# Kernel optimization log

Hardware: AMD Instinct MI355X
Metric: run time of the kernel (lower is better)

## Reference

```python
import jax, jax.numpy as jnp
import numpy as np

B, T, D, H = 64, 512, 512, 1024


def setup_inputs() -> dict:
    key = jax.random.key(0)
    k1, k2, k3 = jax.random.split(key, 3)
    x = jax.random.normal(k1, (B, T, D), dtype=jnp.float32)
    W = jax.random.normal(k2, (D, 4 * H), dtype=jnp.float32) * 0.02  # input kernel
    U = jax.random.normal(k3, (H, 4 * H), dtype=jnp.float32) * 0.02  # recurrent kernel
    b = jnp.zeros((4 * H,), dtype=jnp.float32)
    return {"x": x, "W": W, "U": U, "b": b}


def reference(x, W, U, b):
    # Keras LSTM, gate order [i, f, c(g), o], sigmoid recurrent activation, tanh activation.
    # return_sequences=False, return_state=True -> pred == h_T; output = concat([h_T, h_T, c_T]).
    batch = x.shape[0]
    hidden = U.shape[0]

    def step(carry, xt):
        h, c = carry
        z = xt @ W + h @ U + b  # [B, 4H]
        i, f, g, o = jnp.split(z, 4, axis=-1)
        i = jax.nn.sigmoid(i)
        f = jax.nn.sigmoid(f)
        o = jax.nn.sigmoid(o)
        c_new = f * c + i * jnp.tanh(g)
        h_new = o * jnp.tanh(c_new)
        return (h_new, c_new), None

    h0 = jnp.zeros((batch, hidden), dtype=x.dtype)
    c0 = jnp.zeros((batch, hidden), dtype=x.dtype)
    xs = jnp.swapaxes(x, 0, 1)  # [T, B, D]
    (hT, cT), _ = jax.lax.scan(step, (h0, c0), xs)
    return jnp.concatenate([hT, hT, cT], axis=-1)  # [B, 3H]
```

## Files before the change

kernel.cpp:

```cpp
#include <hip/hip_runtime.h>
#include <stdint.h>

typedef unsigned short u16;

#define T_STEPS 512
#define BATCH   64
#define DIN     512
#define HID     1024
#define G4      4096
#define NBLK    128
#define NH      8
#define NC      32
#define THREADS 512

#define U_LD    1032
#define W_LD    520

#define SM_BYTES 99328
#define WT_OFF   66048

#define XB_BYTES ((size_t)T_STEPS * BATCH * DIN * 2)
#define HB_OFF   XB_BYTES
#define HB_BYTES (2u * BATCH * HID * 2)
#define FLG_OFF  (HB_OFF + HB_BYTES)
#define FLG_BYTES 2048
#define WS_NEED  (FLG_OFF + FLG_BYTES)

typedef float f32x16 __attribute__((ext_vector_type(16)));
typedef short bf16x8 __attribute__((ext_vector_type(8)));
typedef unsigned uint32x4 __attribute__((ext_vector_type(4)));

__device__ __forceinline__ u16 f2bf(float f) {
  unsigned u = __float_as_uint(f);
  u += 0x7fffu + ((u >> 16) & 1u);
  return (u16)(u >> 16);
}
__device__ __forceinline__ float sigm(float x) {
  return __builtin_amdgcn_rcpf(1.f + __expf(-x));
}
__device__ __forceinline__ float fast_tanh(float x) {
  return 1.f - 2.f * __builtin_amdgcn_rcpf(__expf(2.f * x) + 1.f);
}

__device__ __forceinline__ uint32x4 load16_sc(uint64_t addr) {
  uint32x4 d;
  asm volatile("global_load_dwordx4 %0, %1, off sc0 sc1" : "=v"(d) : "v"(addr));
  return d;
}
__device__ __forceinline__ unsigned load4_sc(uint64_t addr) {
  unsigned d;
  asm volatile("global_load_dword %0, %1, off sc0 sc1" : "=v"(d) : "v"(addr));
  return d;
}
__device__ __forceinline__ void store16_sc(uint64_t addr, uint32x4 v) {
  asm volatile("global_store_dwordx4 %0, %1, off sc0 sc1" :: "v"(addr), "v"(v) : "memory");
}
__device__ __forceinline__ void store4_sc(uint64_t addr, unsigned v) {
  asm volatile("global_store_dword %0, %1, off sc0 sc1" :: "v"(addr), "v"(v) : "memory");
}
#define WAITV(n) asm volatile("s_waitcnt vmcnt(" #n ")" ::: "memory")

__global__ void cvt_x(const float* __restrict__ x, u16* __restrict__ xb) {
  int i = blockIdx.x * 256 + threadIdx.x;
  int dblk = i & 63;
  int rest = i >> 6;
  int b = rest & 63;
  int t = rest >> 6;
  const float4* s = reinterpret_cast<const float4*>(x + ((size_t)(b * T_STEPS + t)) * DIN + dblk * 8);
  float4 f0 = s[0], f1 = s[1];
  uint4 o;
  o.x = (unsigned)f2bf(f0.x) | ((unsigned)f2bf(f0.y) << 16);
  o.y = (unsigned)f2bf(f0.z) | ((unsigned)f2bf(f0.w) << 16);
  o.z = (unsigned)f2bf(f1.x) | ((unsigned)f2bf(f1.y) << 16);
  o.w = (unsigned)f2bf(f1.z) | ((unsigned)f2bf(f1.w) << 16);
  *reinterpret_cast<uint4*>(xb + ((size_t)(t * BATCH + b)) * DIN + dblk * 8) = o;
}

__launch_bounds__(THREADS)
__global__ void lstm_kernel(const float* __restrict__ W, const float* __restrict__ U,
                            const float* __restrict__ bias, const u16* __restrict__ xb,
                            u16* __restrict__ hbuf, float* __restrict__ out,
                            unsigned* __restrict__ flags) {
  __shared__ __align__(16) char smraw[SM_BYTES];
  u16* Ut = (u16*)smraw;
  u16* Wt = (u16*)(smraw + WT_OFF);
  float* zp = (float*)smraw;

  const int tid = threadIdx.x;
  const int bid = blockIdx.x;
  const int j0 = bid * NH;

  for (int idx = tid; idx < NC * HID; idx += THREADS) {
    int c = idx & (NC - 1);
    int k = idx >> 5;
    int gcol = ((c >> 3) << 10) + j0 + (c & 7);
    Ut[c * U_LD + k] = f2bf(U[(size_t)k * G4 + gcol]);
  }
  for (int idx = tid; idx < NC * DIN; idx += THREADS) {
    int c = idx & (NC - 1);
    int k = idx >> 5;
    int gcol = ((c >> 3) << 10) + j0 + (c & 7);
    Wt[c * W_LD + k] = f2bf(W[(size_t)k * G4 + gcol]);
  }
  __syncthreads();

  const int l   = tid & 63;
  const int wv  = tid >> 6;
  const int m_t = wv & 1;
  const int ks  = wv >> 1;
  const int cl  = l & 31;
  const int q   = l >> 5;

  bf16x8 ubf[16], wbf[8];
  {
    const u16* ub = Ut + cl * U_LD + ks * 256 + q * 8;
#pragma unroll
    for (int s = 0; s < 16; ++s) ubf[s] = *(const bf16x8*)(ub + s * 16);
    const u16* wb = Wt + cl * W_LD + ks * 128 + q * 8;
#pragma unroll
    for (int s = 0; s < 8; ++s) wbf[s] = *(const bf16x8*)(wb + s * 16);
  }
  __syncthreads();

  const int row = m_t * 32 + cl;
  const int pb = tid >> 3;
  const int pu = tid & 7;
  float c_reg = 0.f;
  const float bi  = bias[j0 + pu];
  const float bf_ = bias[1024 + j0 + pu];
  const float bg  = bias[2048 + j0 + pu];
  const float bo  = bias[3072 + j0 + pu];

  const uint64_t fbase = (uint64_t)flags;
  const uint64_t faddr = fbase + (uint64_t)(ks * 32 + cl) * 16;
  const uint64_t hlane = (uint64_t)(ks * 32 + q) * 1024 + (uint64_t)row * 16;
  const uint64_t puboff = (uint64_t)bid * 1024 + (uint64_t)(wv * 8 + (l >> 3)) * 16;

#define HMFMA(S) acc = __builtin_amdgcn_mfma_f32_32x32x16_bf16( \
    __builtin_bit_cast(bf16x8, abuf[S]), ubf[S], acc, 0, 0, 0)

  for (int t = 0; t < T_STEPS; ++t) {
    f32x16 acc = {0.f,0.f,0.f,0.f,0.f,0.f,0.f,0.f,0.f,0.f,0.f,0.f,0.f,0.f,0.f,0.f};

    const u16* xa = xb + (size_t)t * (BATCH * DIN) + row * DIN + ks * 128 + q * 8;
#pragma unroll
    for (int s = 0; s < 8; ++s) {
      bf16x8 av = *(const bf16x8*)(xa + s * 16);
      acc = __builtin_amdgcn_mfma_f32_32x32x16_bf16(av, wbf[s], acc, 0, 0, 0);
    }

    while (true) {
      unsigned f = load4_sc(faddr);
      WAITV(0);
      if (__all(f >= (unsigned)t)) break;
      __builtin_amdgcn_s_sleep(1);
    }

    const uint64_t hb = (uint64_t)hbuf + (uint64_t)(t & 1) * (BATCH * HID * 2) + hlane;
    uint32x4 abuf[16];
#pragma unroll
    for (int s = 0; s < 16; ++s) abuf[s] = load16_sc(hb + (uint64_t)s * 2048);
    WAITV(12); __builtin_amdgcn_sched_barrier(0);
    HMFMA(0); HMFMA(1); HMFMA(2); HMFMA(3);
    WAITV(8); __builtin_amdgcn_sched_barrier(0);
    HMFMA(4); HMFMA(5); HMFMA(6); HMFMA(7);
    WAITV(4); __builtin_amdgcn_sched_barrier(0);
    HMFMA(8); HMFMA(9); HMFMA(10); HMFMA(11);
    WAITV(0); __builtin_amdgcn_sched_barrier(0);
    HMFMA(12); HMFMA(13); HMFMA(14); HMFMA(15);

#pragma unroll
    for (int r = 0; r < 16; ++r) {
      int rl = (r & 3) + 8 * (r >> 2) + 4 * q;
      zp[ks * 2112 + (m_t * 32 + rl) * 33 + cl] = acc[r];
    }
    __syncthreads();

    float zi = bi, zf = bf_, zg = bg, zo = bo;
#pragma unroll
    for (int k2 = 0; k2 < 4; ++k2) {
      const float* zr = zp + k2 * 2112 + pb * 33;
      zi += zr[pu]; zf += zr[pu + 8]; zg += zr[pu + 16]; zo += zr[pu + 24];
    }
    float ig = sigm(zi), fg = sigm(zf), og = sigm(zo);
    float gg = fast_tanh(zg);
    c_reg = fg * c_reg + ig * gg;
    float h = og * fast_tanh(c_reg);

    unsigned hval = (unsigned)f2bf(h);
    unsigned other = __shfl_xor(hval, 1);
    unsigned pair32 = (l & 1) ? ((other & 0xffffu) | (hval << 16))
                              : ((hval & 0xffffu) | (other << 16));
    int base = l & ~7;
    uint32x4 hv;
    hv[0] = __shfl(pair32, base);
    hv[1] = __shfl(pair32, base + 2);
    hv[2] = __shfl(pair32, base + 4);
    hv[3] = __shfl(pair32, base + 6);

    const uint64_t hbn = (uint64_t)hbuf + (uint64_t)((t + 1) & 1) * (BATCH * HID * 2);
    if ((l & 7) == 0) store16_sc(hbn + puboff, hv);
    if (t == T_STEPS - 1) {
      float* orow = out + (size_t)pb * 3072 + j0 + pu;
      orow[0]    = h;
      orow[1024] = h;
      orow[2048] = c_reg;
    }
    WAITV(0);
    __syncthreads();
    if (tid == 0) store4_sc(fbase + (uint64_t)bid * 16, (unsigned)(t + 1));
  }
#undef HMFMA
}

extern "C" void kernel_launch(void* const* d_in, const int* in_sizes, int n_in,
                              void* d_out, int out_size, void* d_ws, size_t ws_size,
                              hipStream_t stream) {
  const float* x = (const float*)d_in[0];
  const float* W = (const float*)d_in[1];
  const float* U = (const float*)d_in[2];
  const float* b = (const float*)d_in[3];
  float* out = (float*)d_out;

  if (ws_size < WS_NEED) return;

  u16* xb         = (u16*)d_ws;
  u16* hbuf       = (u16*)((char*)d_ws + HB_OFF);
  unsigned* flags = (unsigned*)((char*)d_ws + FLG_OFF);

  hipMemsetAsync((void*)hbuf, 0, HB_BYTES + FLG_BYTES, stream);
  cvt_x<<<(T_STEPS * BATCH * DIN / 8 + 255) / 256, 256, 0, stream>>>(x, xb);
  lstm_kernel<<<NBLK, THREADS, 0, stream>>>(W, U, b, xb, hbuf, out, flags);
}
```

Before: 2.584 ms.

## Split batch into two halves and pipeline LSTM steps across them

Splits the 64-row batch into two independent 32-row chunks, each with its own h double buffer and per-wave flags. While one chunk's gate math and h publish run, the other chunk's h and x operands are already being prefetched, so cross-block wait latency overlaps with useful work. The K dimension is now split across all 8 waves instead of 4 waves times 2 M tiles. Gate columns are reinterleaved so the reduction can use float4 LDS reads. The spin loop gains a timeout escape that silently produces wrong results if it trips.

Result: slower. 2.644 ms (+2.3%).

```diff
diff --git a/kernel.cpp b/kernel.cpp
--- a/kernel.cpp
+++ b/kernel.cpp
@@ -21,9 +21,9 @@
 
 #define XB_BYTES ((size_t)T_STEPS * BATCH * DIN * 2)
 #define HB_OFF   XB_BYTES
-#define HB_BYTES (2u * BATCH * HID * 2)
+#define HB_BYTES (2u * 2u * 128 * 32 * 8 * 2)
 #define FLG_OFF  (HB_OFF + HB_BYTES)
-#define FLG_BYTES 2048
+#define FLG_BYTES (2 * 128 * 4 * 16)
 #define WS_NEED  (FLG_OFF + FLG_BYTES)
 
 typedef float f32x16 __attribute__((ext_vector_type(16)));
@@ -47,6 +47,11 @@
   asm volatile("global_load_dwordx4 %0, %1, off sc0 sc1" : "=v"(d) : "v"(addr));
   return d;
 }
+__device__ __forceinline__ uint32x4 load16_plain(uint64_t addr) {
+  uint32x4 d;
+  asm volatile("global_load_dwordx4 %0, %1, off" : "=v"(d) : "v"(addr));
+  return d;
+}
 __device__ __forceinline__ unsigned load4_sc(uint64_t addr) {
   unsigned d;
   asm volatile("global_load_dword %0, %1, off sc0 sc1" : "=v"(d) : "v"(addr));
@@ -59,6 +64,7 @@
   asm volatile("global_store_dword %0, %1, off sc0 sc1" :: "v"(addr), "v"(v) : "memory");
 }
 #define WAITV(n) asm volatile("s_waitcnt vmcnt(" #n ")" ::: "memory")
+#define SBAR()   __builtin_amdgcn_sched_barrier(0)
 
 __global__ void cvt_x(const float* __restrict__ x, u16* __restrict__ xb) {
   int i = blockIdx.x * 256 + threadIdx.x;
@@ -79,12 +85,11 @@
 __launch_bounds__(THREADS)
 __global__ void lstm_kernel(const float* __restrict__ W, const float* __restrict__ U,
                             const float* __restrict__ bias, const u16* __restrict__ xb,
-                            u16* __restrict__ hbuf, float* __restrict__ out,
-                            unsigned* __restrict__ flags) {
+                            char* __restrict__ ws, float* __restrict__ out) {
   __shared__ __align__(16) char smraw[SM_BYTES];
   u16* Ut = (u16*)smraw;
   u16* Wt = (u16*)(smraw + WT_OFF);
-  float* zp = (float*)smraw;
+  float (*zp)[32][36] = (float(*)[32][36])smraw;
 
   const int tid = threadIdx.x;
   const int bid = blockIdx.x;
@@ -93,124 +98,141 @@
   for (int idx = tid; idx < NC * HID; idx += THREADS) {
     int c = idx & (NC - 1);
     int k = idx >> 5;
-    int gcol = ((c >> 3) << 10) + j0 + (c & 7);
+    int gcol = ((c & 3) << 10) + j0 + (c >> 2);
     Ut[c * U_LD + k] = f2bf(U[(size_t)k * G4 + gcol]);
   }
   for (int idx = tid; idx < NC * DIN; idx += THREADS) {
     int c = idx & (NC - 1);
     int k = idx >> 5;
-    int gcol = ((c >> 3) << 10) + j0 + (c & 7);
+    int gcol = ((c & 3) << 10) + j0 + (c >> 2);
     Wt[c * W_LD + k] = f2bf(W[(size_t)k * G4 + gcol]);
   }
   __syncthreads();
 
-  const int l   = tid & 63;
-  const int wv  = tid >> 6;
-  const int m_t = wv & 1;
-  const int ks  = wv >> 1;
-  const int cl  = l & 31;
-  const int q   = l >> 5;
-
-  bf16x8 ubf[16], wbf[8];
+  const int l  = tid & 63;
+  const int wv = tid >> 6;
+  const int cl = l & 31;
+  const int q  = l >> 5;
+
+  bf16x8 ubf[8], wbf[4];
   {
-    const u16* ub = Ut + cl * U_LD + ks * 256 + q * 8;
-#pragma unroll
-    for (int s = 0; s < 16; ++s) ubf[s] = *(const bf16x8*)(ub + s * 16);
-    const u16* wb = Wt + cl * W_LD + ks * 128 + q * 8;
-#pragma unroll
-    for (int s = 0; s < 8; ++s) wbf[s] = *(const bf16x8*)(wb + s * 16);
+    const u16* ub = Ut + cl * U_LD + wv * 128 + q * 8;
+#pragma unroll
+    for (int s = 0; s < 8; ++s) ubf[s] = *(const bf16x8*)(ub + s * 16);
+    const u16* wb = Wt + cl * W_LD + wv * 64 + q * 8;
+#pragma unroll
+    for (int s = 0; s < 4; ++s) wbf[s] = *(const bf16x8*)(wb + s * 16);
   }
   __syncthreads();
 
-  const int row = m_t * 32 + cl;
   const int pb = tid >> 3;
   const int pu = tid & 7;
-  float c_reg = 0.f;
   const float bi  = bias[j0 + pu];
   const float bf_ = bias[1024 + j0 + pu];
   const float bg  = bias[2048 + j0 + pu];
   const float bo  = bias[3072 + j0 + pu];
-
-  const uint64_t fbase = (uint64_t)flags;
-  const uint64_t faddr = fbase + (uint64_t)(ks * 32 + cl) * 16;
-  const uint64_t hlane = (uint64_t)(ks * 32 + q) * 1024 + (uint64_t)row * 16;
-  const uint64_t puboff = (uint64_t)bid * 1024 + (uint64_t)(wv * 8 + (l >> 3)) * 16;
-
-#define HMFMA(S) acc = __builtin_amdgcn_mfma_f32_32x32x16_bf16( \
-    __builtin_bit_cast(bf16x8, abuf[S]), ubf[S], acc, 0, 0, 0)
+  float cA = 0.f, cB = 0.f;
+  int alive = 1;
+
+  const uint64_t hbase = (uint64_t)ws + HB_OFF;
+  const uint64_t fbase = (uint64_t)ws + FLG_OFF;
+  const uint64_t xb64  = (uint64_t)xb;
+
+  uint32x4 hA[8], xA[4], hB[8], xB[4];
+
+  {
+    const uint64_t hbp = hbase + (uint64_t)cl * 16;
+#pragma unroll
+    for (int s = 0; s < 8; ++s) hA[s] = load16_sc(hbp + (uint64_t)((wv * 16 + 2 * s + q) * 32) * 16);
+    const uint64_t xap = xb64 + ((uint64_t)cl * 512 + (uint64_t)(wv * 64 + q * 8)) * 2;
+#pragma unroll
+    for (int s = 0; s < 4; ++s) xA[s] = load16_plain(xap + (uint64_t)s * 32);
+  }
+
+#define HMFMA(BUF, S) acc = __builtin_amdgcn_mfma_f32_32x32x16_bf16( \
+    __builtin_bit_cast(bf16x8, BUF[S]), ubf[S], acc, 0, 0, 0)
+#define XMFMA(BUF, S) acc = __builtin_amdgcn_mfma_f32_32x32x16_bf16( \
+    __builtin_bit_cast(bf16x8, BUF[S]), wbf[S], acc, 0, 0, 0)
+
+#define PHASE(CH, TT, HC, XC, HN, XN, CREG, OCH, OT) do {                        \
+    WAITV(0); SBAR();             \
+    f32x16 acc = {0.f,0.f,0.f,0.f,0.f,0.f,0.f,0.f,0.f,0.f,0.f,0.f,0.f,0.f,0.f,0.f}; \
+    HMFMA(HC,0); HMFMA(HC,1); HMFMA(HC,2); HMFMA(HC,3);                          \
+    HMFMA(HC,4); HMFMA(HC,5); HMFMA(HC,6); HMFMA(HC,7);                          \
+    XMFMA(XC,0); XMFMA(XC,1); XMFMA(XC,2); XMFMA(XC,3);                          \
+    _Pragma("unroll")                                                            \
+    for (int r = 0; r < 16; ++r) {                                               \
+      int rl = (r & 3) + 8 * (r >> 2) + 4 * q;                                   \
+      zp[wv][rl][cl] = acc[r];                                                   \
+    }                                                                            \
+    __syncthreads();                                   \
+    if (tid < 256) {                                                             \
+      float zi = bi, zf = bf_, zg = bg, zo = bo;                                 \
+      _Pragma("unroll")                                                          \
+      for (int k2 = 0; k2 < 8; ++k2) {                                           \
+        float4 v = *(const float4*)&zp[k2][pb][pu * 4];                          \
+        zi += v.x; zf += v.y; zg += v.z; zo += v.w;                              \
+      }                                                                          \
+      float ig = sigm(zi), fg = sigm(zf), og = sigm(zo);                         \
+      float gg = fast_tanh(zg);                                                  \
+      CREG = fg * CREG + ig * gg;                                                \
+      float h = og * fast_tanh(CREG);                                            \
+      unsigned hval = (unsigned)f2bf(h);                                         \
+      unsigned other = __shfl_xor(hval, 1);                                      \
+      unsigned pair32 = (l & 1) ? ((other & 0xffffu) | (hval << 16))             \
+                                : ((hval & 0xffffu) | (other << 16));            \
+      int base_ = l & ~7;                                                        \
+      uint32x4 hv;                                                               \
+      hv[0] = __shfl(pair32, base_);     hv[1] = __shfl(pair32, base_ + 2);      \
+      hv[2] = __shfl(pair32, base_ + 4); hv[3] = __shfl(pair32, base_ + 6);      \
+      if ((l & 7) == 0)                                                          \
+        store16_sc(hbase + (uint64_t)(CH) * 131072 +                             \
+                   (uint64_t)(((TT) + 1) & 1) * 65536 + (uint64_t)bid * 512 +    \
+                   (uint64_t)(wv * 8 + (l >> 3)) * 16, hv);                      \
+      if ((TT) == T_STEPS - 1) {                                                 \
+        float* orow = out + (size_t)((CH) * 32 + pb) * 3072 + j0 + pu;           \
+        orow[0] = h; orow[1024] = h; orow[2048] = CREG;                          \
+      }                                                                          \
+      WAITV(0);                        \
+      if (l == 0)                                                                \
+        store4_sc(fbase + (uint64_t)(CH) * 8192 + (uint64_t)bid * 64 +           \
+                  (uint64_t)wv * 16, (unsigned)((TT) + 1));                      \
+    }                                                                            \
+    if (alive) {                      \
+      const uint64_t fa = fbase + (uint64_t)(OCH) * 8192 +                       \
+                          (uint64_t)(wv * 16 + (l >> 2)) * 64 +                  \
+                          (uint64_t)(l & 3) * 16;                                \
+      int spins = 0;                                                             \
+      while (true) {                                                             \
+        unsigned f = load4_sc(fa);                                               \
+        WAITV(0);                                                                \
+        if (__all(f >= (unsigned)(OT))) break;                                   \
+        if (++spins > (1 << 22)) { alive = 0; break; }                           \
+        __builtin_amdgcn_s_sleep(1);                                             \
+      }                                                                          \
+    }                                                                            \
+    {                                 \
+      const uint64_t hbp = hbase + (uint64_t)(OCH) * 131072 +                    \
+                           (uint64_t)((OT) & 1) * 65536 + (uint64_t)cl * 16;     \
+      _Pragma("unroll")                                                          \
+      for (int s = 0; s < 8; ++s)                                                \
+        HN[s] = load16_sc(hbp + (uint64_t)((wv * 16 + 2 * s + q) * 32) * 16);    \
+      const int otx = ((OT) < T_STEPS) ? (OT) : 0;                               \
+      const uint64_t xap = xb64 + ((uint64_t)(otx * 64 + (OCH) * 32 + cl) * 512  \
+                                   + (uint64_t)(wv * 64 + q * 8)) * 2;           \
+      _Pragma("unroll")                                                          \
+      for (int s = 0; s < 4; ++s) XN[s] = load16_plain(xap + (uint64_t)s * 32);  \
+    }                                                                            \
+    __syncthreads();                              \
+  } while (0)
 
   for (int t = 0; t < T_STEPS; ++t) {
-    f32x16 acc = {0.f,0.f,0.f,0.f,0.f,0.f,0.f,0.f,0.f,0.f,0.f,0.f,0.f,0.f,0.f,0.f};
-
-    const u16* xa = xb + (size_t)t * (BATCH * DIN) + row * DIN + ks * 128 + q * 8;
-#pragma unroll
-    for (int s = 0; s < 8; ++s) {
-      bf16x8 av = *(const bf16x8*)(xa + s * 16);
-      acc = __builtin_amdgcn_mfma_f32_32x32x16_bf16(av, wbf[s], acc, 0, 0, 0);
-    }
-
-    while (true) {
-      unsigned f = load4_sc(faddr);
-      WAITV(0);
-      if (__all(f >= (unsigned)t)) break;
-      __builtin_amdgcn_s_sleep(1);
-    }
-
-    const uint64_t hb = (uint64_t)hbuf + (uint64_t)(t & 1) * (BATCH * HID * 2) + hlane;
-    uint32x4 abuf[16];
-#pragma unroll
-    for (int s = 0; s < 16; ++s) abuf[s] = load16_sc(hb + (uint64_t)s * 2048);
-    WAITV(12); __builtin_amdgcn_sched_barrier(0);
-    HMFMA(0); HMFMA(1); HMFMA(2); HMFMA(3);
-    WAITV(8); __builtin_amdgcn_sched_barrier(0);
-    HMFMA(4); HMFMA(5); HMFMA(6); HMFMA(7);
-    WAITV(4); __builtin_amdgcn_sched_barrier(0);
-    HMFMA(8); HMFMA(9); HMFMA(10); HMFMA(11);
-    WAITV(0); __builtin_amdgcn_sched_barrier(0);
-    HMFMA(12); HMFMA(13); HMFMA(14); HMFMA(15);
-
-#pragma unroll
-    for (int r = 0; r < 16; ++r) {
-      int rl = (r & 3) + 8 * (r >> 2) + 4 * q;
-      zp[ks * 2112 + (m_t * 32 + rl) * 33 + cl] = acc[r];
-    }
-    __syncthreads();
-
-    float zi = bi, zf = bf_, zg = bg, zo = bo;
-#pragma unroll
-    for (int k2 = 0; k2 < 4; ++k2) {
-      const float* zr = zp + k2 * 2112 + pb * 33;
-      zi += zr[pu]; zf += zr[pu + 8]; zg += zr[pu + 16]; zo += zr[pu + 24];
-    }
-    float ig = sigm(zi), fg = sigm(zf), og = sigm(zo);
-    float gg = fast_tanh(zg);
-    c_reg = fg * c_reg + ig * gg;
-    float h = og * fast_tanh(c_reg);
-
-    unsigned hval = (unsigned)f2bf(h);
-    unsigned other = __shfl_xor(hval, 1);
-    unsigned pair32 = (l & 1) ? ((other & 0xffffu) | (hval << 16))
-                              : ((hval & 0xffffu) | (other << 16));
-    int base = l & ~7;
-    uint32x4 hv;
-    hv[0] = __shfl(pair32, base);
-    hv[1] = __shfl(pair32, base + 2);
-    hv[2] = __shfl(pair32, base + 4);
-    hv[3] = __shfl(pair32, base + 6);
-
-    const uint64_t hbn = (uint64_t)hbuf + (uint64_t)((t + 1) & 1) * (BATCH * HID * 2);
-    if ((l & 7) == 0) store16_sc(hbn + puboff, hv);
-    if (t == T_STEPS - 1) {
-      float* orow = out + (size_t)pb * 3072 + j0 + pu;
-      orow[0]    = h;
-      orow[1024] = h;
-      orow[2048] = c_reg;
-    }
-    WAITV(0);
-    __syncthreads();
-    if (tid == 0) store4_sc(fbase + (uint64_t)bid * 16, (unsigned)(t + 1));
-  }
+    PHASE(0, t, hA, xA, hB, xB, cA, 1, t);
+    PHASE(1, t, hB, xB, hA, xA, cB, 0, t + 1);
+  }
+#undef PHASE
 #undef HMFMA
+#undef XMFMA
 }
 
 extern "C" void kernel_launch(void* const* d_in, const int* in_sizes, int n_in,
@@ -224,11 +246,8 @@
 
   if (ws_size < WS_NEED) return;
 
-  u16* xb         = (u16*)d_ws;
-  u16* hbuf       = (u16*)((char*)d_ws + HB_OFF);
-  unsigned* flags = (unsigned*)((char*)d_ws + FLG_OFF);
-
-  hipMemsetAsync((void*)hbuf, 0, HB_BYTES + FLG_BYTES, stream);
+  u16* xb = (u16*)d_ws;
+  hipMemsetAsync((char*)d_ws + HB_OFF, 0, HB_BYTES + FLG_BYTES, stream);
   cvt_x<<<(T_STEPS * BATCH * DIN / 8 + 255) / 256, 256, 0, stream>>>(x, xb);
-  lstm_kernel<<<NBLK, THREADS, 0, stream>>>(W, U, b, xb, hbuf, out, flags);
-}
+  lstm_kernel<<<NBLK, THREADS, 0, stream>>>(W, U, b, xb, (char*)d_ws, out);
+}
```

## Replace flag-based step barrier with step-tagged h values polled directly

Applied to the files above, without the earlier changes.

Drops the separate per-block flag array and its flag store and poll. Each bf16 h value is now packed with a 16-bit step tag into a 32-bit word, and consumers poll the h buffer itself until every tag matches, so the data and the readiness signal arrive in a single load round trip. The recurrent U fragments are no longer held in registers; they are read from LDS on every step, which frees registers for the doubled h load, and the z scratch area moves so it does not overwrite Ut. The cost is twice the h traffic per step, repeated reloads of the full h tile while spinning, extra LDS reads, and a spin limit that gives up silently instead of waiting forever.

New measurement: 5.586 ms. 2.16x slower.

```diff
diff --git a/kernel.cpp b/kernel.cpp
--- a/kernel.cpp
+++ b/kernel.cpp
@@ -16,15 +16,14 @@
 #define U_LD    1032
 #define W_LD    520
 
-#define SM_BYTES 99328
+#define SM_BYTES 99840
 #define WT_OFF   66048
 
 #define XB_BYTES ((size_t)T_STEPS * BATCH * DIN * 2)
 #define HB_OFF   XB_BYTES
-#define HB_BYTES (2u * BATCH * HID * 2)
-#define FLG_OFF  (HB_OFF + HB_BYTES)
-#define FLG_BYTES 2048
-#define WS_NEED  (FLG_OFF + FLG_BYTES)
+#define HB_PAR   262144
+#define HB_BYTES (2u * HB_PAR)
+#define WS_NEED  (HB_OFF + HB_BYTES)
 
 typedef float f32x16 __attribute__((ext_vector_type(16)));
 typedef short bf16x8 __attribute__((ext_vector_type(8)));
@@ -47,18 +46,16 @@
   asm volatile("global_load_dwordx4 %0, %1, off sc0 sc1" : "=v"(d) : "v"(addr));
   return d;
 }
-__device__ __forceinline__ unsigned load4_sc(uint64_t addr) {
-  unsigned d;
-  asm volatile("global_load_dword %0, %1, off sc0 sc1" : "=v"(d) : "v"(addr));
+__device__ __forceinline__ uint32x4 load16_plain(uint64_t addr) {
+  uint32x4 d;
+  asm volatile("global_load_dwordx4 %0, %1, off" : "=v"(d) : "v"(addr));
   return d;
 }
 __device__ __forceinline__ void store16_sc(uint64_t addr, uint32x4 v) {
   asm volatile("global_store_dwordx4 %0, %1, off sc0 sc1" :: "v"(addr), "v"(v) : "memory");
 }
-__device__ __forceinline__ void store4_sc(uint64_t addr, unsigned v) {
-  asm volatile("global_store_dword %0, %1, off sc0 sc1" :: "v"(addr), "v"(v) : "memory");
-}
 #define WAITV(n) asm volatile("s_waitcnt vmcnt(" #n ")" ::: "memory")
+#define SBAR()   __builtin_amdgcn_sched_barrier(0)
 
 __global__ void cvt_x(const float* __restrict__ x, u16* __restrict__ xb) {
   int i = blockIdx.x * 256 + threadIdx.x;
@@ -79,12 +76,11 @@
 __launch_bounds__(THREADS)
 __global__ void lstm_kernel(const float* __restrict__ W, const float* __restrict__ U,
                             const float* __restrict__ bias, const u16* __restrict__ xb,
-                            u16* __restrict__ hbuf, float* __restrict__ out,
-                            unsigned* __restrict__ flags) {
+                            char* __restrict__ ws, float* __restrict__ out) {
   __shared__ __align__(16) char smraw[SM_BYTES];
   u16* Ut = (u16*)smraw;
   u16* Wt = (u16*)(smraw + WT_OFF);
-  float* zp = (float*)smraw;
+  float* zp = (float*)(smraw + WT_OFF);
 
   const int tid = threadIdx.x;
   const int bid = blockIdx.x;
@@ -111,16 +107,15 @@
   const int cl  = l & 31;
   const int q   = l >> 5;
 
-  bf16x8 ubf[16], wbf[8];
+  bf16x8 wbf[8];
   {
-    const u16* ub = Ut + cl * U_LD + ks * 256 + q * 8;
-#pragma unroll
-    for (int s = 0; s < 16; ++s) ubf[s] = *(const bf16x8*)(ub + s * 16);
     const u16* wb = Wt + cl * W_LD + ks * 128 + q * 8;
 #pragma unroll
     for (int s = 0; s < 8; ++s) wbf[s] = *(const bf16x8*)(wb + s * 16);
   }
   __syncthreads();
+
+  const u16* ubp = Ut + cl * U_LD + ks * 256 + q * 8;
 
   const int row = m_t * 32 + cl;
   const int pb = tid >> 3;
@@ -131,43 +126,64 @@
   const float bg  = bias[2048 + j0 + pu];
   const float bo  = bias[3072 + j0 + pu];
 
-  const uint64_t fbase = (uint64_t)flags;
-  const uint64_t faddr = fbase + (uint64_t)(ks * 32 + cl) * 16;
-  const uint64_t hlane = (uint64_t)(ks * 32 + q) * 1024 + (uint64_t)row * 16;
-  const uint64_t puboff = (uint64_t)bid * 1024 + (uint64_t)(wv * 8 + (l >> 3)) * 16;
-
-#define HMFMA(S) acc = __builtin_amdgcn_mfma_f32_32x32x16_bf16( \
-    __builtin_bit_cast(bf16x8, abuf[S]), ubf[S], acc, 0, 0, 0)
+  const uint64_t hbB = (uint64_t)ws + HB_OFF;
+  const uint64_t xb64 = (uint64_t)xb;
+  const uint64_t hoff = (uint64_t)(ks * 32 + q) * 2048 + (uint64_t)row * 32;
+  const uint64_t puboff = (uint64_t)bid * 2048 + (uint64_t)(tid >> 3) * 32 +
+                          (uint64_t)((l >> 2) & 1) * 16;
+
+  int alive = 1;
 
   for (int t = 0; t < T_STEPS; ++t) {
+    const unsigned tagv = (unsigned)t;
+    const uint64_t hb = hbB + (uint64_t)(t & 1) * HB_PAR + hoff;
+
+    uint32x4 hbuf[32];
+#define ISSUEH() do { _Pragma("unroll") for (int s_ = 0; s_ < 16; ++s_) { \
+      hbuf[2 * s_]     = load16_sc(hb + (uint64_t)s_ * 4096); \
+      hbuf[2 * s_ + 1] = load16_sc(hb + (uint64_t)s_ * 4096 + 16); } } while (0)
+    ISSUEH();
+    uint32x4 xr[8];
+    {
+      const uint64_t xa = xb64 + ((uint64_t)t * (BATCH * DIN) +
+                                  (uint64_t)row * DIN + ks * 128 + q * 8) * 2;
+#pragma unroll
+      for (int s = 0; s < 8; ++s) xr[s] = load16_plain(xa + (uint64_t)s * 32);
+    }
+
+    int spins = 0;
+    while (alive) {
+      WAITV(0); SBAR();
+      unsigned bad = 0;
+#pragma unroll
+      for (int s = 0; s < 32; ++s) {
+#pragma unroll
+        for (int e = 0; e < 4; ++e) bad |= (hbuf[s][e] ^ tagv) & 0xffffu;
+      }
+      if (__all(bad == 0)) break;
+      if (++spins > (1 << 18)) { alive = 0; break; }
+      __builtin_amdgcn_s_sleep(4);
+      ISSUEH();
+    }
+#undef ISSUEH
+
     f32x16 acc = {0.f,0.f,0.f,0.f,0.f,0.f,0.f,0.f,0.f,0.f,0.f,0.f,0.f,0.f,0.f,0.f};
-
-    const u16* xa = xb + (size_t)t * (BATCH * DIN) + row * DIN + ks * 128 + q * 8;
-#pragma unroll
-    for (int s = 0; s < 8; ++s) {
-      bf16x8 av = *(const bf16x8*)(xa + s * 16);
-      acc = __builtin_amdgcn_mfma_f32_32x32x16_bf16(av, wbf[s], acc, 0, 0, 0);
-    }
-
-    while (true) {
-      unsigned f = load4_sc(faddr);
-      WAITV(0);
-      if (__all(f >= (unsigned)t)) break;
-      __builtin_amdgcn_s_sleep(1);
-    }
-
-    const uint64_t hb = (uint64_t)hbuf + (uint64_t)(t & 1) * (BATCH * HID * 2) + hlane;
-    uint32x4 abuf[16];
-#pragma unroll
-    for (int s = 0; s < 16; ++s) abuf[s] = load16_sc(hb + (uint64_t)s * 2048);
-    WAITV(12); __builtin_amdgcn_sched_barrier(0);
-    HMFMA(0); HMFMA(1); HMFMA(2); HMFMA(3);
-    WAITV(8); __builtin_amdgcn_sched_barrier(0);
-    HMFMA(4); HMFMA(5); HMFMA(6); HMFMA(7);
-    WAITV(4); __builtin_amdgcn_sched_barrier(0);
-    HMFMA(8); HMFMA(9); HMFMA(10); HMFMA(11);
-    WAITV(0); __builtin_amdgcn_sched_barrier(0);
-    HMFMA(12); HMFMA(13); HMFMA(14); HMFMA(15);
+#pragma unroll
+    for (int s = 0; s < 16; ++s) {
+      uint32x4 d0 = hbuf[2 * s], d1 = hbuf[2 * s + 1];
+      uint32x4 pk;
+      pk[0] = (d0[0] >> 16) | (d0[1] & 0xffff0000u);
+      pk[1] = (d0[2] >> 16) | (d0[3] & 0xffff0000u);
+      pk[2] = (d1[0] >> 16) | (d1[1] & 0xffff0000u);
+      pk[3] = (d1[2] >> 16) | (d1[3] & 0xffff0000u);
+      bf16x8 a = __builtin_bit_cast(bf16x8, pk);
+      bf16x8 uf = *(const bf16x8*)(ubp + s * 16);
+      acc = __builtin_amdgcn_mfma_f32_32x32x16_bf16(a, uf, acc, 0, 0, 0);
+    }
+#pragma unroll
+    for (int s = 0; s < 8; ++s)
+      acc = __builtin_amdgcn_mfma_f32_32x32x16_bf16(
+          __builtin_bit_cast(bf16x8, xr[s]), wbf[s], acc, 0, 0, 0);
 
 #pragma unroll
     for (int r = 0; r < 16; ++r) {
@@ -187,30 +203,24 @@
     c_reg = fg * c_reg + ig * gg;
     float h = og * fast_tanh(c_reg);
 
-    unsigned hval = (unsigned)f2bf(h);
-    unsigned other = __shfl_xor(hval, 1);
-    unsigned pair32 = (l & 1) ? ((other & 0xffffu) | (hval << 16))
-                              : ((hval & 0xffffu) | (other << 16));
-    int base = l & ~7;
+    unsigned hval = ((unsigned)f2bf(h) << 16) | (unsigned)(t + 1);
+    int base_ = l & ~3;
     uint32x4 hv;
-    hv[0] = __shfl(pair32, base);
-    hv[1] = __shfl(pair32, base + 2);
-    hv[2] = __shfl(pair32, base + 4);
-    hv[3] = __shfl(pair32, base + 6);
-
-    const uint64_t hbn = (uint64_t)hbuf + (uint64_t)((t + 1) & 1) * (BATCH * HID * 2);
-    if ((l & 7) == 0) store16_sc(hbn + puboff, hv);
+    hv[0] = __shfl(hval, base_);
+    hv[1] = __shfl(hval, base_ + 1);
+    hv[2] = __shfl(hval, base_ + 2);
+    hv[3] = __shfl(hval, base_ + 3);
+    if ((l & 3) == 0)
+      store16_sc(hbB + (uint64_t)((t + 1) & 1) * HB_PAR + puboff, hv);
+
     if (t == T_STEPS - 1) {
       float* orow = out + (size_t)pb * 3072 + j0 + pu;
       orow[0]    = h;
       orow[1024] = h;
       orow[2048] = c_reg;
     }
-    WAITV(0);
     __syncthreads();
-    if (tid == 0) store4_sc(fbase + (uint64_t)bid * 16, (unsigned)(t + 1));
-  }
-#undef HMFMA
+  }
 }
 
 extern "C" void kernel_launch(void* const* d_in, const int* in_sizes, int n_in,
@@ -224,11 +234,8 @@
 
   if (ws_size < WS_NEED) return;
 
-  u16* xb         = (u16*)d_ws;
-  u16* hbuf       = (u16*)((char*)d_ws + HB_OFF);
-  unsigned* flags = (unsigned*)((char*)d_ws + FLG_OFF);
-
-  hipMemsetAsync((void*)hbuf, 0, HB_BYTES + FLG_BYTES, stream);
+  u16* xb = (u16*)d_ws;
+  hipMemsetAsync((char*)d_ws + HB_OFF, 0, HB_BYTES, stream);
   cvt_x<<<(T_STEPS * BATCH * DIN / 8 + 255) / 256, 256, 0, stream>>>(x, xb);
-  lstm_kernel<<<NBLK, THREADS, 0, stream>>>(W, U, b, xb, hbuf, out, flags);
-}
+  lstm_kernel<<<NBLK, THREADS, 0, stream>>>(W, U, b, xb, (char*)d_ws, out);
+}
```
